# Kernel optimization log

Hardware: AMD Instinct MI355X
Metric: run time of the kernel (lower is better)

The kernel has to match this reference:

```python
import jax, jax.numpy as jnp
import numpy as np

N = 100000
E = 1600000
D_IN = 128
D_HID = 128
D_OUT = 64


def setup_inputs() -> dict:
    key = jax.random.key(0)
    ks = jax.random.split(key, 12)
    x = jax.random.normal(ks[0], (N, D_IN), dtype=jnp.float32)
    src = jax.random.randint(ks[1], (E,), 0, N, dtype=jnp.int32)
    dst = jax.random.randint(ks[2], (E,), 0, N, dtype=jnp.int32)
    def lin(k, din, dout):
        s = 1.0 / np.sqrt(din)
        return jax.random.uniform(k, (din, dout), jnp.float32, -s, s)
    return {
        "x": x, "src": src, "dst": dst,
        "Ws0": lin(ks[3], D_IN, D_HID), "Wn0": lin(ks[4], D_IN, D_HID), "b0": jnp.zeros((D_HID,), jnp.float32),
        "Ws1": lin(ks[5], D_HID, D_HID), "Wn1": lin(ks[6], D_HID, D_HID), "b1": jnp.zeros((D_HID,), jnp.float32),
        "Ws2": lin(ks[7], D_HID, D_OUT), "Wn2": lin(ks[8], D_HID, D_OUT), "b2": jnp.zeros((D_OUT,), jnp.float32),
    }


def _sage_conv(h, src, dst, Ws, Wn, b):
    # mean aggregation of neighbor (src) features onto dst nodes
    deg = jax.ops.segment_sum(jnp.ones((src.shape[0],), h.dtype), dst, num_segments=N)
    agg = jax.ops.segment_sum(h[src], dst, num_segments=N)  # [N, d_in]
    mean = agg / jnp.maximum(deg, 1.0)[:, None]
    return h @ Ws + mean @ Wn + b


def reference(x, src, dst, Ws0, Wn0, b0, Ws1, Wn1, b1, Ws2, Wn2, b2):
    h = _sage_conv(x, src, dst, Ws0, Wn0, b0)
    h = jax.nn.relu(h)  # dropout is identity in eval mode
    h = _sage_conv(h, src, dst, Ws1, Wn1, b1)
    h = jax.nn.relu(h)
    h = _sage_conv(h, src, dst, Ws2, Wn2, b2)
    return h
```

## Files before the change

### kernel.cpp

```cpp
#include <hip/hip_runtime.h>

#define NN 100000
#define NE 1600000
#define DF 128
#define TS 136
#define NCB 391
#define NWA 256
#define SZA 6250
#define NH (NCB * NWA)
#define CAPB 6144

typedef unsigned int uint32;
typedef unsigned short u16;
typedef _Float16 f16;
typedef f16 f16x8 __attribute__((ext_vector_type(8)));
typedef f16 f16x2 __attribute__((ext_vector_type(2)));
typedef float f32x4 __attribute__((ext_vector_type(4)));

__device__ __forceinline__ uint32 pk2(float a, float b) {
    union { f16x2 h; uint32 u; } v;
    v.h.x = (f16)a; v.h.y = (f16)b;
    return v.u;
}
__device__ __forceinline__ u16 f2h(float a) {
    union { f16 h; u16 u; } v; v.h = (f16)a; return v.u;
}


__global__ __launch_bounds__(256) void histA_prep(
    const int* __restrict__ dst, int* __restrict__ H, int* __restrict__ CBT,
    const float* __restrict__ Ws0, const float* __restrict__ Wn0,
    const float* __restrict__ Ws1, const float* __restrict__ Wn1,
    const float* __restrict__ Ws2, const float* __restrict__ Wn2,
    u16* __restrict__ WB,
    const float* __restrict__ x, uint2* __restrict__ xh) {
    __shared__ int lh[NCB];
    int b = blockIdx.x, t = threadIdx.x;
    if (b < NWA) {
        int w = b;
        for (int i = t; i < NCB; i += 256) lh[i] = 0;
        __syncthreads();
        int e0 = w * SZA, e1 = min(e0 + SZA, NE);
        for (int e = e0 + t; e < e1; e += 256) atomicAdd(&lh[dst[e] >> 8], 1);
        __syncthreads();
        for (int i = t; i < NCB; i += 256) {
            int v = lh[i];
            H[i * NWA + w] = v;
            if (v) atomicAdd(&CBT[i], v);
        }
    } else if (b < NWA + 320) {
        int u = (b - NWA) * 256 + t;
        if (u < 65536) {
            int m = u >> 14;
            int local = u & 16383;
            int k = local >> 7, n = local & 127;
            const float* W = (m == 0) ? Ws0 : (m == 1) ? Wn0 : (m == 2) ? Ws1 : Wn1;
            WB[m * 16384 + n * 128 + k] = f2h(W[k * 128 + n]);
        } else {
            int local = u - 65536;
            int half = local >> 13;
            int idx = local & 8191;
            int k = idx >> 6, n = idx & 63;
            const float* W = half ? Wn2 : Ws2;
            WB[4 * 16384 + (n + half * 64) * 128 + k] = f2h(W[k * 64 + n]);
        }
    } else {
        int u = (b - NWA - 320) * 256 + t;
        if (u < NN * DF / 4) {
            float4 v = ((const float4*)x)[u];
            uint2 o;
            o.x = pk2(v.x, v.y);
            o.y = pk2(v.z, v.w);
            xh[u] = o;
        }
    }
}

__global__ __launch_bounds__(512) void scanCBW(const int* __restrict__ CBT,
                                               const int* __restrict__ H,
                                               int* __restrict__ O,
                                               int* __restrict__ rowptr) {
    __shared__ int sm[512];
    __shared__ int sh[256];
    int cb = blockIdx.x, t = threadIdx.x;
    int v = (t < NCB) ? CBT[t] : 0;
    sm[t] = v;
    __syncthreads();
    for (int off = 1; off < 512; off <<= 1) {
        int x = (t >= off) ? sm[t - off] : 0;
        __syncthreads();
        sm[t] += x;
        __syncthreads();
    }
    if (cb == 0 && t == NCB - 1) {
        O[NH] = sm[t];
        rowptr[NN] = sm[t];
    }
    int cbo = sm[cb] - CBT[cb];
    int hv = (t < 256) ? H[cb * NWA + t] : 0;
    if (t < 256) sh[t] = hv;
    __syncthreads();
    for (int off = 1; off < 256; off <<= 1) {
        int x = (t >= off && t < 256) ? sh[t - off] : 0;
        __syncthreads();
        if (t < 256) sh[t] += x;
        __syncthreads();
    }
    if (t < 256) O[cb * NWA + t] = cbo + sh[t] - hv;
}

__global__ __launch_bounds__(1024) void passA(const int* __restrict__ src,
                                              const int* __restrict__ dst,
                                              const int* __restrict__ O,
                                              uint32* __restrict__ ebuf) {
    __shared__ int cur[NCB];
    int w = blockIdx.x, t = threadIdx.x;
    for (int i = t; i < NCB; i += 1024) cur[i] = O[i * NWA + w];
    __syncthreads();
    int e0 = w * SZA, e1 = min(e0 + SZA, NE);
    for (int e = e0 + t; e < e1; e += 1024) {
        int d = dst[e];
        int cb = d >> 8;
        int p = atomicAdd(&cur[cb], 1);
        ebuf[p] = ((uint32)src[e] << 8) | (uint32)(d & 255);
    }
}

__global__ __launch_bounds__(256) void passB(const uint32* __restrict__ ebuf,
                                             const int* __restrict__ O,
                                             int* __restrict__ rowptr,
                                             int* __restrict__ col) {
    __shared__ int hist[256], start[256], cur[256];
    __shared__ int seg[CAPB];
    int cb = blockIdx.x, t = threadIdx.x;
    int base = O[cb * NWA], end = O[(cb + 1) * NWA];
    int m = end - base;
    hist[t] = 0;
    __syncthreads();
    for (int i = t; i < m; i += 256) atomicAdd(&hist[ebuf[base + i] & 255], 1);
    __syncthreads();
    int v = hist[t];
    cur[t] = v;
    __syncthreads();
    for (int off = 1; off < 256; off <<= 1) {
        int x = (t >= off) ? cur[t - off] : 0;
        __syncthreads();
        cur[t] += x;
        __syncthreads();
    }
    start[t] = cur[t] - v;
    __syncthreads();
    int node = cb * 256 + t;
    if (node < NN) rowptr[node] = base + start[t];
    cur[t] = start[t];
    __syncthreads();
    if (m <= CAPB) {
        for (int i = t; i < m; i += 256) {
            uint32 u = ebuf[base + i];
            int p = atomicAdd(&cur[u & 255], 1);
            seg[p] = (int)(u >> 8);
        }
        __syncthreads();
        for (int i = t; i < m; i += 256) col[base + i] = seg[i];
    } else {
        for (int i = t; i < m; i += 256) {
            uint32 u = ebuf[base + i];
            int p = atomicAdd(&cur[u & 255], 1);
            col[base + p] = (int)(u >> 8);
        }
    }
}

__global__ __launch_bounds__(256) void gather_f16(const u16* __restrict__ hb,
                                                  const int* __restrict__ rowptr,
                                                  const int* __restrict__ col,
                                                  u16* __restrict__ mean) {
    int bid = blockIdx.x;
    int panel = bid & 1;
    int node = (bid >> 1) * 32 + (threadIdx.x >> 3);
    int g = threadIdx.x & 7;
    const u16* hp = hb + panel * 64 + g * 8;
    int s = rowptr[node], e = rowptr[node + 1];
    float acc[8];
#pragma unroll
    for (int i = 0; i < 8; ++i) acc[i] = 0.f;
    int j = s;
    for (; j + 7 < e; j += 8) {
        int n0 = col[j],     n1 = col[j + 1], n2 = col[j + 2], n3 = col[j + 3];
        int n4 = col[j + 4], n5 = col[j + 5], n6 = col[j + 6], n7 = col[j + 7];
        f16x8 v0 = *(const f16x8*)(hp + (size_t)n0 * DF);
        f16x8 v1 = *(const f16x8*)(hp + (size_t)n1 * DF);
        f16x8 v2 = *(const f16x8*)(hp + (size_t)n2 * DF);
        f16x8 v3 = *(const f16x8*)(hp + (size_t)n3 * DF);
        f16x8 v4 = *(const f16x8*)(hp + (size_t)n4 * DF);
        f16x8 v5 = *(const f16x8*)(hp + (size_t)n5 * DF);
        f16x8 v6 = *(const f16x8*)(hp + (size_t)n6 * DF);
        f16x8 v7 = *(const f16x8*)(hp + (size_t)n7 * DF);
        f16x8 sA = (v0 + v1) + (v2 + v3);
        f16x8 sB = (v4 + v5) + (v6 + v7);
#pragma unroll
        for (int i = 0; i < 8; ++i) acc[i] += (float)sA[i] + (float)sB[i];
    }
    for (; j + 3 < e; j += 4) {
        int n0 = col[j], n1 = col[j + 1], n2 = col[j + 2], n3 = col[j + 3];
        f16x8 v0 = *(const f16x8*)(hp + (size_t)n0 * DF);
        f16x8 v1 = *(const f16x8*)(hp + (size_t)n1 * DF);
        f16x8 v2 = *(const f16x8*)(hp + (size_t)n2 * DF);
        f16x8 v3 = *(const f16x8*)(hp + (size_t)n3 * DF);
        f16x8 sv = (v0 + v1) + (v2 + v3);
#pragma unroll
        for (int i = 0; i < 8; ++i) acc[i] += (float)sv[i];
    }
    for (; j < e; ++j) {
        f16x8 v = *(const f16x8*)(hp + (size_t)col[j] * DF);
#pragma unroll
        for (int i = 0; i < 8; ++i) acc[i] += (float)v[i];
    }
    float invd = 1.f / fmaxf((float)(e - s), 1.f);
    union { f16x8 h; uint4 u; } o;
#pragma unroll
    for (int i = 0; i < 8; ++i) o.h[i] = (f16)(acc[i] * invd);
    *(uint4*)(mean + (size_t)node * DF + panel * 64 + g * 8) = o.u;
}

__global__ __launch_bounds__(256) void gather_add_f16(const u16* __restrict__ gb,
                                                      const u16* __restrict__ selfb,
                                                      const int* __restrict__ rowptr,
                                                      const int* __restrict__ col,
                                                      float* __restrict__ out) {
    int node = blockIdx.x * 32 + (threadIdx.x >> 3);
    int g = threadIdx.x & 7;
    int s = rowptr[node], e = rowptr[node + 1];
    float acc[8];
#pragma unroll
    for (int i = 0; i < 8; ++i) acc[i] = 0.f;
    int j = s;
    for (; j + 7 < e; j += 8) {
        int n0 = col[j],     n1 = col[j + 1], n2 = col[j + 2], n3 = col[j + 3];
        int n4 = col[j + 4], n5 = col[j + 5], n6 = col[j + 6], n7 = col[j + 7];
        f16x8 v0 = *(const f16x8*)(gb + (size_t)n0 * 64 + g * 8);
        f16x8 v1 = *(const f16x8*)(gb + (size_t)n1 * 64 + g * 8);
        f16x8 v2 = *(const f16x8*)(gb + (size_t)n2 * 64 + g * 8);
        f16x8 v3 = *(const f16x8*)(gb + (size_t)n3 * 64 + g * 8);
        f16x8 v4 = *(const f16x8*)(gb + (size_t)n4 * 64 + g * 8);
        f16x8 v5 = *(const f16x8*)(gb + (size_t)n5 * 64 + g * 8);
        f16x8 v6 = *(const f16x8*)(gb + (size_t)n6 * 64 + g * 8);
        f16x8 v7 = *(const f16x8*)(gb + (size_t)n7 * 64 + g * 8);
        f16x8 sA = (v0 + v1) + (v2 + v3);
        f16x8 sB = (v4 + v5) + (v6 + v7);
#pragma unroll
        for (int i = 0; i < 8; ++i) acc[i] += (float)sA[i] + (float)sB[i];
    }
    for (; j + 3 < e; j += 4) {
        int n0 = col[j], n1 = col[j + 1], n2 = col[j + 2], n3 = col[j + 3];
        f16x8 v0 = *(const f16x8*)(gb + (size_t)n0 * 64 + g * 8);
        f16x8 v1 = *(const f16x8*)(gb + (size_t)n1 * 64 + g * 8);
        f16x8 v2 = *(const f16x8*)(gb + (size_t)n2 * 64 + g * 8);
        f16x8 v3 = *(const f16x8*)(gb + (size_t)n3 * 64 + g * 8);
        f16x8 sv = (v0 + v1) + (v2 + v3);
#pragma unroll
        for (int i = 0; i < 8; ++i) acc[i] += (float)sv[i];
    }
    for (; j < e; ++j) {
        f16x8 v = *(const f16x8*)(gb + (size_t)col[j] * 64 + g * 8);
#pragma unroll
        for (int i = 0; i < 8; ++i) acc[i] += (float)v[i];
    }
    float invd = 1.f / fmaxf((float)(e - s), 1.f);
    f16x8 sv = *(const f16x8*)(selfb + (size_t)node * 64 + g * 8);
    float4 a, b;
    a.x = (float)sv[0] + acc[0] * invd; a.y = (float)sv[1] + acc[1] * invd;
    a.z = (float)sv[2] + acc[2] * invd; a.w = (float)sv[3] + acc[3] * invd;
    b.x = (float)sv[4] + acc[4] * invd; b.y = (float)sv[5] + acc[5] * invd;
    b.z = (float)sv[6] + acc[6] * invd; b.w = (float)sv[7] + acc[7] * invd;
    float4* op = (float4*)(out + (size_t)node * 64 + g * 8);
    op[0] = a; op[1] = b;
}

__device__ __forceinline__ void stage_a(u16* sm, const u16* g, int row0, int tid) {
#pragma unroll
    for (int i = 0; i < 8; ++i) {
        int idx = i * 256 + tid;
        int r = idx >> 4, c = (idx & 15) * 8;
        uint4 v = make_uint4(0, 0, 0, 0);
        int gr = row0 + r;
        if (gr < NN) v = *(const uint4*)(g + (size_t)gr * DF + c);
        *(uint4*)(sm + r * TS + c) = v;
    }
}

__device__ __forceinline__ void stage_w128(u16* sm, const u16* wt, int tid) {
#pragma unroll
    for (int i = 0; i < 8; ++i) {
        int idx = i * 256 + tid;
        int r = idx >> 4, c = (idx & 15) * 8;
        *(uint4*)(sm + r * TS + c) = *(const uint4*)(wt + (size_t)r * 128 + c);
    }
}

__device__ __forceinline__ f16x8 frag(const u16* sm, int row, int lane, int kc) {
    return *(const f16x8*)(sm + (row + (lane & 15)) * TS + kc * 32 + (lane >> 4) * 8);
}

__device__ __forceinline__ void mfma8(const u16* As, const u16* Bs, int wrow, int lane,
                                      f32x4 acc[2][8]) {
    f16x8 a[2][4];
#pragma unroll
    for (int rt = 0; rt < 2; ++rt)
#pragma unroll
        for (int kc = 0; kc < 4; ++kc) a[rt][kc] = frag(As, wrow + rt * 16, lane, kc);
#pragma unroll
    for (int n = 0; n < 8; ++n) {
#pragma unroll
        for (int kc = 0; kc < 4; ++kc) {
            f16x8 b = frag(Bs, n * 16, lane, kc);
            acc[0][n] = __builtin_amdgcn_mfma_f32_16x16x32_f16(a[0][kc], b, acc[0][n], 0, 0, 0);
            acc[1][n] = __builtin_amdgcn_mfma_f32_16x16x32_f16(a[1][kc], b, acc[1][n], 0, 0, 0);
        }
    }
}

__global__ __launch_bounds__(256) void gemm_sage_f16(
    const u16* H, const u16* M,
    const u16* __restrict__ Ws, const u16* __restrict__ Wn,
    const float* __restrict__ bias, u16* OutH) {
    __shared__ u16 As[128 * TS];
    __shared__ u16 Bs[128 * TS];
    const int tid = threadIdx.x;
    const int lane = tid & 63;
    const int wrow = (tid >> 6) * 32;
    const int row0 = blockIdx.x * 128;

    f32x4 acc[2][8];
#pragma unroll
    for (int rt = 0; rt < 2; ++rt)
#pragma unroll
        for (int n = 0; n < 8; ++n) acc[rt][n] = {0.f, 0.f, 0.f, 0.f};

    stage_a(As, H, row0, tid);
    stage_w128(Bs, Ws, tid);
    __syncthreads();
    mfma8(As, Bs, wrow, lane, acc);
    __syncthreads();
    stage_a(As, M, row0, tid);
    stage_w128(Bs, Wn, tid);
    __syncthreads();
    mfma8(As, Bs, wrow, lane, acc);

    const int cit = lane & 15;
    const int rq = (lane >> 4) * 4;
#pragma unroll
    for (int rt = 0; rt < 2; ++rt)
#pragma unroll
        for (int n = 0; n < 8; ++n) {
            float bv = bias[n * 16 + cit];
            f32x4 v = acc[rt][n];
#pragma unroll
            for (int r = 0; r < 4; ++r) {
                int gr = row0 + wrow + rt * 16 + rq + r;
                if (gr < NN) {
                    float o = fmaxf(v[r] + bv, 0.f);
                    OutH[(size_t)gr * DF + n * 16 + cit] = f2h(o);
                }
            }
        }
}

__global__ __launch_bounds__(256) void gemm_l2_f16(
    const u16* __restrict__ H, const u16* __restrict__ W2,
    const float* __restrict__ b2, u16* __restrict__ selfb, u16* __restrict__ g2) {
    __shared__ u16 As[128 * TS];
    __shared__ u16 Bs[128 * TS];
    const int tid = threadIdx.x;
    const int lane = tid & 63;
    const int wrow = (tid >> 6) * 32;
    const int row0 = blockIdx.x * 128;

    f32x4 acc[2][8];
#pragma unroll
    for (int rt = 0; rt < 2; ++rt)
#pragma unroll
        for (int n = 0; n < 8; ++n) acc[rt][n] = {0.f, 0.f, 0.f, 0.f};

    stage_a(As, H, row0, tid);
    stage_w128(Bs, W2, tid);
    __syncthreads();
    mfma8(As, Bs, wrow, lane, acc);

    const int cit = lane & 15;
    const int rq = (lane >> 4) * 4;
#pragma unroll
    for (int rt = 0; rt < 2; ++rt)
#pragma unroll
        for (int n = 0; n < 8; ++n) {
            f32x4 v = acc[rt][n];
            float bv = (n < 4) ? b2[n * 16 + cit] : 0.f;
#pragma unroll
            for (int r = 0; r < 4; ++r) {
                int gr = row0 + wrow + rt * 16 + rq + r;
                if (gr < NN) {
                    if (n < 4) selfb[(size_t)gr * 64 + n * 16 + cit] = f2h(v[r] + bv);
                    else g2[(size_t)gr * 64 + (n - 4) * 16 + cit] = f2h(v[r]);
                }
            }
        }
}

extern "C" void kernel_launch(void* const* d_in, const int* in_sizes, int n_in,
                              void* d_out, int out_size, void* d_ws, size_t ws_size,
                              hipStream_t stream) {
    const float* x   = (const float*)d_in[0];
    const int*   src = (const int*)d_in[1];
    const int*   dst = (const int*)d_in[2];
    const float* Ws0 = (const float*)d_in[3];
    const float* Wn0 = (const float*)d_in[4];
    const float* b0  = (const float*)d_in[5];
    const float* Ws1 = (const float*)d_in[6];
    const float* Wn1 = (const float*)d_in[7];
    const float* b1  = (const float*)d_in[8];
    const float* Ws2 = (const float*)d_in[9];
    const float* Wn2 = (const float*)d_in[10];
    const float* b2  = (const float*)d_in[11];
    float* out = (float*)d_out;

    int* H       = (int*)d_ws;
    int* O       = H + NH;
    int* CBT     = O + 100352;
    int* CBO     = CBT + 512;
    int* rowptr  = CBO + 512;
    int* col     = rowptr + 100352;
    uint32* ebuf = (uint32*)(col + NE);
    u16* WB      = (u16*)(ebuf + NE);
    u16* W0s = WB, *W0n = WB + 16384, *W1s = WB + 2 * 16384, *W1n = WB + 3 * 16384;
    u16* W2  = WB + 4 * 16384;
    u16* P1 = WB + 5 * 16384;
    u16* P3 = P1 + (size_t)NN * DF;
    u16* G2   = P3;
    u16* SELF = P3 + (size_t)NN * 64;

    const int gB = (NN + 127) / 128;

    hipMemsetAsync(CBT, 0, NCB * sizeof(int), stream);
    histA_prep<<<NWA + 320 + NN * DF / 4 / 256, 256, 0, stream>>>(
        dst, H, CBT, Ws0, Wn0, Ws1, Wn1, Ws2, Wn2, WB, x, (uint2*)P1);

    scanCBW<<<NCB, 512, 0, stream>>>(CBT, H, O, rowptr);
    passA<<<NWA, 1024, 0, stream>>>(src, dst, O, ebuf);
    passB<<<NCB, 256, 0, stream>>>(ebuf, O, rowptr, col);

    gather_f16<<<(NN / 32) * 2, 256, 0, stream>>>(P1, rowptr, col, P3);
    gemm_sage_f16<<<gB, 256, 0, stream>>>(P1, P3, W0s, W0n, b0, P1);

    gather_f16<<<(NN / 32) * 2, 256, 0, stream>>>(P1, rowptr, col, P3);
    gemm_sage_f16<<<gB, 256, 0, stream>>>(P1, P3, W1s, W1n, b1, P1);

    gemm_l2_f16<<<gB, 256, 0, stream>>>(P1, W2, b2, SELF, G2);
    gather_add_f16<<<NN / 32, 256, 0, stream>>>(G2, SELF, rowptr, col, out);
}
```

Before: 374.5 us.

## Stage GEMM tiles with direct global-to-LDS loads, XOR swizzle and split weights

```diff
diff --git a/kernel.cpp b/kernel.cpp
--- a/kernel.cpp
+++ b/kernel.cpp
@@ -3,7 +3,6 @@
 #define NN 100000
 #define NE 1600000
 #define DF 128
-#define TS 136
 #define NCB 391
 #define NWA 256
 #define SZA 6250
@@ -277,45 +276,56 @@
     op[0] = a; op[1] = b;
 }
 
-__device__ __forceinline__ void stage_a(u16* sm, const u16* g, int row0, int tid) {
+__device__ __forceinline__ void gl_lds16(const u16* g, u16* l) {
+    __builtin_amdgcn_global_load_lds(
+        (const __attribute__((address_space(1))) void*)g,
+        (__attribute__((address_space(3))) void*)l, 16, 0, 0);
+}
+
+__device__ __forceinline__ void stage128(u16* lds, const u16* g, int tid) {
+    int lane = tid & 63, wid = tid >> 6;
 #pragma unroll
     for (int i = 0; i < 8; ++i) {
-        int idx = i * 256 + tid;
-        int r = idx >> 4, c = (idx & 15) * 8;
-        uint4 v = make_uint4(0, 0, 0, 0);
-        int gr = row0 + r;
-        if (gr < NN) v = *(const uint4*)(g + (size_t)gr * DF + c);
-        *(uint4*)(sm + r * TS + c) = v;
-    }
-}
-
-__device__ __forceinline__ void stage_w128(u16* sm, const u16* wt, int tid) {
-#pragma unroll
-    for (int i = 0; i < 8; ++i) {
-        int idx = i * 256 + tid;
-        int r = idx >> 4, c = (idx & 15) * 8;
-        *(uint4*)(sm + r * TS + c) = *(const uint4*)(wt + (size_t)r * 128 + c);
-    }
-}
-
-__device__ __forceinline__ f16x8 frag(const u16* sm, int row, int lane, int kc) {
-    return *(const f16x8*)(sm + (row + (lane & 15)) * TS + kc * 32 + (lane >> 4) * 8);
-}
-
-__device__ __forceinline__ void mfma8(const u16* As, const u16* Bs, int wrow, int lane,
-                                      f32x4 acc[2][8]) {
-    f16x8 a[2][4];
+        int r4 = (wid + i * 4) * 4;
+        int row = r4 + (lane >> 4);
+        int c = lane & 15;
+        gl_lds16(g + (size_t)row * 128 + ((c ^ (row & 7)) * 8), lds + r4 * 128);
+    }
+}
+
+__device__ __forceinline__ void stage64(u16* lds, const u16* g, int tid) {
+    int lane = tid & 63, wid = tid >> 6;
+#pragma unroll
+    for (int i = 0; i < 4; ++i) {
+        int r4 = (wid + i * 4) * 4;
+        int row = r4 + (lane >> 4);
+        int c = lane & 15;
+        gl_lds16(g + (size_t)row * 128 + ((c ^ (row & 7)) * 8), lds + r4 * 128);
+    }
+}
+
+__device__ __forceinline__ f16x8 fragS(const u16* sm, int row, int lane, int kc) {
+    int r = row + (lane & 15);
+    int c = (kc * 4 + (lane >> 4)) ^ (r & 7);
+    return *(const f16x8*)(sm + r * 128 + c * 8);
+}
+
+__device__ __forceinline__ void loadA(f16x8 a[2][4], const u16* As, int wrow, int lane) {
 #pragma unroll
     for (int rt = 0; rt < 2; ++rt)
 #pragma unroll
-        for (int kc = 0; kc < 4; ++kc) a[rt][kc] = frag(As, wrow + rt * 16, lane, kc);
-#pragma unroll
-    for (int n = 0; n < 8; ++n) {
+        for (int kc = 0; kc < 4; ++kc) a[rt][kc] = fragS(As, wrow + rt * 16, lane, kc);
+}
+
+__device__ __forceinline__ void mfmaH(const f16x8 a[2][4], const u16* Bs, int lane,
+                                      f32x4 acc[2][8], int nb) {
+#pragma unroll
+    for (int n = 0; n < 4; ++n) {
 #pragma unroll
         for (int kc = 0; kc < 4; ++kc) {
-            f16x8 b = frag(Bs, n * 16, lane, kc);
-            acc[0][n] = __builtin_amdgcn_mfma_f32_16x16x32_f16(a[0][kc], b, acc[0][n], 0, 0, 0);
-            acc[1][n] = __builtin_amdgcn_mfma_f32_16x16x32_f16(a[1][kc], b, acc[1][n], 0, 0, 0);
+            f16x8 b = fragS(Bs, n * 16, lane, kc);
+            acc[0][nb + n] = __builtin_amdgcn_mfma_f32_16x16x32_f16(a[0][kc], b, acc[0][nb + n], 0, 0, 0);
+            acc[1][nb + n] = __builtin_amdgcn_mfma_f32_16x16x32_f16(a[1][kc], b, acc[1][nb + n], 0, 0, 0);
         }
     }
 }
@@ -324,8 +334,8 @@
     const u16* H, const u16* M,
     const u16* __restrict__ Ws, const u16* __restrict__ Wn,
     const float* __restrict__ bias, u16* OutH) {
-    __shared__ u16 As[128 * TS];
-    __shared__ u16 Bs[128 * TS];
+    __shared__ u16 As[128 * 128];
+    __shared__ u16 Bs[64 * 128];
     const int tid = threadIdx.x;
     const int lane = tid & 63;
     const int wrow = (tid >> 6) * 32;
@@ -336,16 +346,27 @@
     for (int rt = 0; rt < 2; ++rt)
 #pragma unroll
         for (int n = 0; n < 8; ++n) acc[rt][n] = {0.f, 0.f, 0.f, 0.f};
-
-    stage_a(As, H, row0, tid);
-    stage_w128(Bs, Ws, tid);
-    __syncthreads();
-    mfma8(As, Bs, wrow, lane, acc);
-    __syncthreads();
-    stage_a(As, M, row0, tid);
-    stage_w128(Bs, Wn, tid);
-    __syncthreads();
-    mfma8(As, Bs, wrow, lane, acc);
+    f16x8 a[2][4];
+
+    stage128(As, H + (size_t)row0 * 128, tid);
+    stage64(Bs, Ws, tid);
+    __syncthreads();
+    loadA(a, As, wrow, lane);
+    mfmaH(a, Bs, lane, acc, 0);
+    __syncthreads();
+    stage64(Bs, Ws + 64 * 128, tid);
+    __syncthreads();
+    mfmaH(a, Bs, lane, acc, 4);
+    __syncthreads();
+    stage128(As, M + (size_t)row0 * 128, tid);
+    stage64(Bs, Wn, tid);
+    __syncthreads();
+    loadA(a, As, wrow, lane);
+    mfmaH(a, Bs, lane, acc, 0);
+    __syncthreads();
+    stage64(Bs, Wn + 64 * 128, tid);
+    __syncthreads();
+    mfmaH(a, Bs, lane, acc, 4);
 
     const int cit = lane & 15;
     const int rq = (lane >> 4) * 4;
@@ -369,8 +390,8 @@
 __global__ __launch_bounds__(256) void gemm_l2_f16(
     const u16* __restrict__ H, const u16* __restrict__ W2,
     const float* __restrict__ b2, u16* __restrict__ selfb, u16* __restrict__ g2) {
-    __shared__ u16 As[128 * TS];
-    __shared__ u16 Bs[128 * TS];
+    __shared__ u16 As[128 * 128];
+    __shared__ u16 Bs[64 * 128];
     const int tid = threadIdx.x;
     const int lane = tid & 63;
     const int wrow = (tid >> 6) * 32;
@@ -381,11 +402,17 @@
     for (int rt = 0; rt < 2; ++rt)
 #pragma unroll
         for (int n = 0; n < 8; ++n) acc[rt][n] = {0.f, 0.f, 0.f, 0.f};
-
-    stage_a(As, H, row0, tid);
-    stage_w128(Bs, W2, tid);
-    __syncthreads();
-    mfma8(As, Bs, wrow, lane, acc);
+    f16x8 a[2][4];
+
+    stage128(As, H + (size_t)row0 * 128, tid);
+    stage64(Bs, W2, tid);
+    __syncthreads();
+    loadA(a, As, wrow, lane);
+    mfmaH(a, Bs, lane, acc, 0);
+    __syncthreads();
+    stage64(Bs, W2 + 64 * 128, tid);
+    __syncthreads();
+    mfmaH(a, Bs, lane, acc, 4);
 
     const int cit = lane & 15;
     const int rq = (lane >> 4) * 4;
```

Measured after the change: 371.4 us. No clear change (-0.8%).
